# Optimization experiments

Hardware: AMD Instinct MI355X
Metric: run time of the kernel (lower is better)

The kernel has to match this reference:

```python
import jax, jax.numpy as jnp
import numpy as np

N_SIDE = 14          # ViT-S/16 on 224x224 -> 14x14 patches
D_BACKBONE = 384
D_MODEL = 512
B_CLIPS = 32
T_FRAMES = 64
BT = B_CLIPS * T_FRAMES
LN_EPS = 1e-5


def setup_inputs() -> dict:
    key = jax.random.key(0)
    k0, k1, k2, k3, k4 = jax.random.split(key, 5)
    patch_tokens = jax.random.normal(k0, (BT, N_SIDE * N_SIDE, D_BACKBONE), dtype=jnp.float32)
    raw = jax.random.uniform(k1, (BT, 4), dtype=jnp.float32)
    # make well-formed boxes: x1<=x2, y1<=y2 (module clamps anyway)
    xy1 = jnp.minimum(raw[:, :2], raw[:, 2:])
    xy2 = jnp.maximum(raw[:, :2], raw[:, 2:])
    bboxes = jnp.concatenate([xy1, xy2], axis=1)
    obj_visible = jax.random.bernoulli(k2, 0.9, (BT,)).astype(jnp.float32)
    W = jax.random.normal(k3, (D_BACKBONE, D_MODEL), dtype=jnp.float32) * 0.02
    b = jnp.zeros((D_MODEL,), dtype=jnp.float32)
    gamma = jnp.ones((D_MODEL,), dtype=jnp.float32)
    beta = jnp.zeros((D_MODEL,), dtype=jnp.float32)
    mask_token = jax.random.normal(k4, (1, D_MODEL), dtype=jnp.float32) * 0.02
    return {"patch_tokens": patch_tokens, "bboxes": bboxes, "obj_visible": obj_visible,
            "B": B_CLIPS, "T": T_FRAMES, "W": W, "b": b, "gamma": gamma, "beta": beta,
            "mask_token": mask_token}


def _roi_mean_pool(patch_tokens, bboxes):
    bt, N, D = patch_tokens.shape
    n = N_SIDE
    grid = patch_tokens.reshape(bt, n, n, D)
    # exact replica of torch index math (clamp -> trunc/ceil -> clamp -> max)
    x1 = jnp.clip(bboxes[:, 0] * n, 0, n - 1).astype(jnp.int32)
    y1 = jnp.clip(bboxes[:, 1] * n, 0, n - 1).astype(jnp.int32)
    x2 = jnp.clip(jnp.ceil(jnp.clip(bboxes[:, 2] * n, 0, n)), 1, n).astype(jnp.int32)
    y2 = jnp.clip(jnp.ceil(jnp.clip(bboxes[:, 3] * n, 0, n)), 1, n).astype(jnp.int32)
    x2 = jnp.maximum(x2, x1 + 1)
    y2 = jnp.maximum(y2, y1 + 1)
    idx = jnp.arange(n)
    my = (idx[None, :] >= y1[:, None]) & (idx[None, :] < y2[:, None])  # [BT, n]
    mx = (idx[None, :] >= x1[:, None]) & (idx[None, :] < x2[:, None])  # [BT, n]
    mask = (my[:, :, None] & mx[:, None, :]).astype(grid.dtype)        # [BT, n, n]
    count = ((y2 - y1) * (x2 - x1)).astype(grid.dtype)                 # >= 1 always
    pooled = jnp.einsum('bhw,bhwd->bd', mask, grid) / count[:, None]
    return pooled


def reference(patch_tokens, bboxes, obj_visible, B, T, W, b, gamma, beta, mask_token):
    pooled = _roi_mean_pool(patch_tokens, bboxes)          # [BT, D_backbone]
    out = pooled @ W + b                                   # [BT, d_model]
    mu = jnp.mean(out, axis=-1, keepdims=True)
    var = jnp.mean(jnp.square(out - mu), axis=-1, keepdims=True)
    out = (out - mu) * jax.lax.rsqrt(var + LN_EPS) * gamma + beta
    vis = obj_visible[:, None]
    out = vis * out + (1.0 - vis) * mask_token             # learnable mask token blend
    return out.reshape(B, T, -1)
```

## Files before the change

kernel.cpp:

```cpp
#include <hip/hip_runtime.h>
#include <hip/hip_bf16.h>

#define N_SIDE 14
#define N_PATCH (N_SIDE * N_SIDE)
#define D_BB 384
#define DQ_BB (D_BB / 4)
#define D_MODEL 512
#define CQ (D_MODEL / 4)
#define BT_TOTAL 2048
#define LN_EPS 1e-5f
#define ROWS 8
#define KP 4
#define KCHUNK (D_BB / KP)
#define GROUPS 8

__device__ __forceinline__ void fma4(float4& a, float s, const float4& wv) {
    a.x = fmaf(s, wv.x, a.x);
    a.y = fmaf(s, wv.y, a.y);
    a.z = fmaf(s, wv.z, a.z);
    a.w = fmaf(s, wv.w, a.w);
}

__global__ __launch_bounds__(768) void pool_kernel(
    const float* __restrict__ patch,
    const float* __restrict__ bboxes,
    float* __restrict__ pooled)
{
    const int bt = blockIdx.x;
    const int t  = threadIdx.x;
    const int qd = t % DQ_BB;
    const int g  = t / DQ_BB;

    const float bx1 = bboxes[bt * 4 + 0];
    const float by1 = bboxes[bt * 4 + 1];
    const float bx2 = bboxes[bt * 4 + 2];
    const float by2 = bboxes[bt * 4 + 3];

    int x1 = (int)fminf(fmaxf(bx1 * (float)N_SIDE, 0.f), (float)(N_SIDE - 1));
    int y1 = (int)fminf(fmaxf(by1 * (float)N_SIDE, 0.f), (float)(N_SIDE - 1));
    int x2 = (int)fminf(fmaxf(ceilf(fminf(fmaxf(bx2 * (float)N_SIDE, 0.f), (float)N_SIDE)), 1.f), (float)N_SIDE);
    int y2 = (int)fminf(fmaxf(ceilf(fminf(fmaxf(by2 * (float)N_SIDE, 0.f), (float)N_SIDE)), 1.f), (float)N_SIDE);
    x2 = max(x2, x1 + 1);
    y2 = max(y2, y1 + 1);

    const int wd = x2 - x1;
    const int ht = y2 - y1;
    const int total = wd * ht;
    const float inv_count = 1.f / (float)total;
    const float inv_wd = 1.f / (float)wd;
    const int cell0 = y1 * N_SIDE + x1;

    const float4* __restrict__ base = (const float4*)patch + (size_t)bt * N_PATCH * DQ_BB + qd;

    auto cell_off = [&](int c) -> size_t {
        const int y = (int)(((float)c + 0.5f) * inv_wd);
        const int x = c - y * wd;
        return (size_t)(cell0 + y * N_SIDE + x) * DQ_BB;
    };

    float4 acc = make_float4(0.f, 0.f, 0.f, 0.f);
    int c = g;
    for (; c + 3 * GROUPS < total; c += 4 * GROUPS) {
        const float4 v0 = base[cell_off(c)];
        const float4 v1 = base[cell_off(c + GROUPS)];
        const float4 v2 = base[cell_off(c + 2 * GROUPS)];
        const float4 v3 = base[cell_off(c + 3 * GROUPS)];
        acc.x += (v0.x + v1.x) + (v2.x + v3.x);
        acc.y += (v0.y + v1.y) + (v2.y + v3.y);
        acc.z += (v0.z + v1.z) + (v2.z + v3.z);
        acc.w += (v0.w + v1.w) + (v2.w + v3.w);
    }
    for (; c < total; c += GROUPS) {
        const float4 v = base[cell_off(c)];
        acc.x += v.x; acc.y += v.y; acc.z += v.z; acc.w += v.w;
    }

    __shared__ float4 part[GROUPS][DQ_BB];
    part[g][qd] = acc;
    __syncthreads();

    if (t < DQ_BB) {
        float4 s = part[0][t];
#pragma unroll
        for (int p = 1; p < GROUPS; ++p) {
            const float4 v = part[p][t];
            s.x += v.x; s.y += v.y; s.z += v.z; s.w += v.w;
        }
        s.x *= inv_count; s.y *= inv_count; s.z *= inv_count; s.w *= inv_count;
        ((float4*)pooled)[(size_t)bt * DQ_BB + t] = s;
    }
}

__global__ __launch_bounds__(512) void gemm_ln_kernel(
    const float* __restrict__ pooled,
    const float* __restrict__ W,
    const float* __restrict__ bias,
    const float* __restrict__ gamma,
    const float* __restrict__ beta,
    const float* __restrict__ mask_tok,
    const float* __restrict__ vis,
    float* __restrict__ out)
{
    const int tid  = threadIdx.x;
    const int part = tid >> 7;
    const int jq   = tid & 127;
    const int r0   = blockIdx.x * ROWS;

    __shared__ float sp[ROWS][D_BB];
    __shared__ float red[KP - 1][32][CQ];
    __shared__ float lnred[2][ROWS][2];

    {
        const float4* p4  = (const float4*)(pooled + (size_t)r0 * D_BB);
        float4*       sp4 = (float4*)sp;
        for (int i = tid; i < ROWS * DQ_BB; i += 512) sp4[i] = p4[i];
    }
    __syncthreads();

    const float4* Wq = (const float4*)W;
    float4 acc[ROWS];
#pragma unroll
    for (int r = 0; r < ROWS; ++r) acc[r] = make_float4(0.f, 0.f, 0.f, 0.f);

    const int dbase = part * KCHUNK;
#pragma unroll 2
    for (int i = 0; i < KCHUNK / 4; ++i) {
        const int d = dbase + i * 4;
        const float4 w0 = Wq[(size_t)(d + 0) * CQ + jq];
        const float4 w1 = Wq[(size_t)(d + 1) * CQ + jq];
        const float4 w2 = Wq[(size_t)(d + 2) * CQ + jq];
        const float4 w3 = Wq[(size_t)(d + 3) * CQ + jq];
#pragma unroll
        for (int r = 0; r < ROWS; ++r) {
            const float4 a = *(const float4*)&sp[r][d];
            fma4(acc[r], a.x, w0);
            fma4(acc[r], a.y, w1);
            fma4(acc[r], a.z, w2);
            fma4(acc[r], a.w, w3);
        }
    }

    if (part != 0) {
#pragma unroll
        for (int r = 0; r < ROWS; ++r) {
            red[part - 1][r * 4 + 0][jq] = acc[r].x;
            red[part - 1][r * 4 + 1][jq] = acc[r].y;
            red[part - 1][r * 4 + 2][jq] = acc[r].z;
            red[part - 1][r * 4 + 3][jq] = acc[r].w;
        }
    }
    __syncthreads();

    if (part == 0) {
#pragma unroll
        for (int p = 0; p < KP - 1; ++p) {
#pragma unroll
            for (int r = 0; r < ROWS; ++r) {
                acc[r].x += red[p][r * 4 + 0][jq];
                acc[r].y += red[p][r * 4 + 1][jq];
                acc[r].z += red[p][r * 4 + 2][jq];
                acc[r].w += red[p][r * 4 + 3][jq];
            }
        }
        const float4 bj = ((const float4*)bias)[jq];
#pragma unroll
        for (int r = 0; r < ROWS; ++r) {
            acc[r].x += bj.x; acc[r].y += bj.y; acc[r].z += bj.z; acc[r].w += bj.w;
        }

        const int lane = tid & 63;
        const int wv   = tid >> 6;
#pragma unroll
        for (int r = 0; r < ROWS; ++r) {
            float s  = acc[r].x + acc[r].y + acc[r].z + acc[r].w;
            float s2 = acc[r].x * acc[r].x + acc[r].y * acc[r].y +
                       acc[r].z * acc[r].z + acc[r].w * acc[r].w;
#pragma unroll
            for (int off = 32; off >= 1; off >>= 1) {
                s  += __shfl_xor(s,  off);
                s2 += __shfl_xor(s2, off);
            }
            if (lane == 0) { lnred[wv][r][0] = s; lnred[wv][r][1] = s2; }
        }
    }
    __syncthreads();

    if (part == 0) {
        const float4 g4 = ((const float4*)gamma)[jq];
        const float4 b4 = ((const float4*)beta)[jq];
        const float4 m4 = ((const float4*)mask_tok)[jq];
#pragma unroll
        for (int r = 0; r < ROWS; ++r) {
            const float s    = lnred[0][r][0] + lnred[1][r][0];
            const float s2   = lnred[0][r][1] + lnred[1][r][1];
            const float mean = s * (1.f / (float)D_MODEL);
            const float var  = s2 * (1.f / (float)D_MODEL) - mean * mean;
            const float rstd = rsqrtf(var + LN_EPS);
            const float v    = vis[r0 + r];
            const float iv   = 1.f - v;
            float4 o;
            o.x = v * ((acc[r].x - mean) * rstd * g4.x + b4.x) + iv * m4.x;
            o.y = v * ((acc[r].y - mean) * rstd * g4.y + b4.y) + iv * m4.y;
            o.z = v * ((acc[r].z - mean) * rstd * g4.z + b4.z) + iv * m4.z;
            o.w = v * ((acc[r].w - mean) * rstd * g4.w + b4.w) + iv * m4.w;
            ((float4*)out)[(size_t)(r0 + r) * CQ + jq] = o;
        }
    }
}

extern "C" void kernel_launch(void* const* d_in, const int* in_sizes, int n_in,
                              void* d_out, int out_size, void* d_ws, size_t ws_size,
                              hipStream_t stream) {
    const float* patch  = (const float*)d_in[0];
    const float* bboxes = (const float*)d_in[1];
    const float* vis    = (const float*)d_in[2];
    const float* W      = (const float*)d_in[5];
    const float* bias   = (const float*)d_in[6];
    const float* gamma  = (const float*)d_in[7];
    const float* beta   = (const float*)d_in[8];
    const float* mtok   = (const float*)d_in[9];

    float* pooled = (float*)d_ws;
    float* out    = (float*)d_out;

    pool_kernel<<<BT_TOTAL, 768, 0, stream>>>(patch, bboxes, pooled);
    gemm_ln_kernel<<<BT_TOTAL / ROWS, 512, 0, stream>>>(
        pooled, W, bias, gamma, beta, mtok, vis, out);
}
```

Before: 37.68 us.

## Split ROI pooling across two blocks per box with atomic accumulation

Each box's pooling is now spread over two 384-thread blocks instead of one 768-thread block. The partial sums are combined with float atomicAdd into a workspace that is zeroed by a memset first. The division by the cell count moves into the GEMM+LayerNorm epilogue, which recomputes the box size. The aim is finer-grained scheduling, at the cost of an extra memset launch, atomic traffic, and summation order that is no longer deterministic.

```diff
diff --git a/kernel.cpp b/kernel.cpp
--- a/kernel.cpp
+++ b/kernel.cpp
@@ -12,7 +12,9 @@
 #define ROWS 8
 #define KP 4
 #define KCHUNK (D_BB / KP)
-#define GROUPS 8
+#define GROUPS 4
+#define SPLIT 2
+#define ESTRIDE (GROUPS * SPLIT)
 
 __device__ __forceinline__ void fma4(float4& a, float s, const float4& wv) {
     a.x = fmaf(s, wv.x, a.x);
@@ -21,32 +23,37 @@
     a.w = fmaf(s, wv.w, a.w);
 }
 
-__global__ __launch_bounds__(768) void pool_kernel(
+__device__ __forceinline__ void box_params(const float* __restrict__ bboxes, int bt,
+                                           int& x1, int& y1, int& wd, int& total) {
+    const float bx1 = bboxes[bt * 4 + 0];
+    const float by1 = bboxes[bt * 4 + 1];
+    const float bx2 = bboxes[bt * 4 + 2];
+    const float by2 = bboxes[bt * 4 + 3];
+    x1 = (int)fminf(fmaxf(bx1 * (float)N_SIDE, 0.f), (float)(N_SIDE - 1));
+    y1 = (int)fminf(fmaxf(by1 * (float)N_SIDE, 0.f), (float)(N_SIDE - 1));
+    int x2 = (int)fminf(fmaxf(ceilf(fminf(fmaxf(bx2 * (float)N_SIDE, 0.f), (float)N_SIDE)), 1.f), (float)N_SIDE);
+    int y2 = (int)fminf(fmaxf(ceilf(fminf(fmaxf(by2 * (float)N_SIDE, 0.f), (float)N_SIDE)), 1.f), (float)N_SIDE);
+    x2 = max(x2, x1 + 1);
+    y2 = max(y2, y1 + 1);
+    wd = x2 - x1;
+    total = wd * (y2 - y1);
+}
+
+__global__ __launch_bounds__(384) void pool_kernel(
     const float* __restrict__ patch,
     const float* __restrict__ bboxes,
     float* __restrict__ pooled)
 {
-    const int bt = blockIdx.x;
-    const int t  = threadIdx.x;
-    const int qd = t % DQ_BB;
-    const int g  = t / DQ_BB;
-
-    const float bx1 = bboxes[bt * 4 + 0];
-    const float by1 = bboxes[bt * 4 + 1];
-    const float bx2 = bboxes[bt * 4 + 2];
-    const float by2 = bboxes[bt * 4 + 3];
-
-    int x1 = (int)fminf(fmaxf(bx1 * (float)N_SIDE, 0.f), (float)(N_SIDE - 1));
-    int y1 = (int)fminf(fmaxf(by1 * (float)N_SIDE, 0.f), (float)(N_SIDE - 1));
-    int x2 = (int)fminf(fmaxf(ceilf(fminf(fmaxf(bx2 * (float)N_SIDE, 0.f), (float)N_SIDE)), 1.f), (float)N_SIDE);
-    int y2 = (int)fminf(fmaxf(ceilf(fminf(fmaxf(by2 * (float)N_SIDE, 0.f), (float)N_SIDE)), 1.f), (float)N_SIDE);
-    x2 = max(x2, x1 + 1);
-    y2 = max(y2, y1 + 1);
-
-    const int wd = x2 - x1;
-    const int ht = y2 - y1;
-    const int total = wd * ht;
-    const float inv_count = 1.f / (float)total;
+    const int bid = blockIdx.x;
+    const int bt  = bid >> 1;
+    const int s   = bid & 1;
+    const int t   = threadIdx.x;
+    const int qd  = t % DQ_BB;
+    const int g   = t / DQ_BB;
+    const int e   = s * GROUPS + g;
+
+    int x1, y1, wd, total;
+    box_params(bboxes, bt, x1, y1, wd, total);
     const float inv_wd = 1.f / (float)wd;
     const int cell0 = y1 * N_SIDE + x1;
 
@@ -59,18 +66,18 @@
     };
 
     float4 acc = make_float4(0.f, 0.f, 0.f, 0.f);
-    int c = g;
-    for (; c + 3 * GROUPS < total; c += 4 * GROUPS) {
+    int c = e;
+    for (; c + 3 * ESTRIDE < total; c += 4 * ESTRIDE) {
         const float4 v0 = base[cell_off(c)];
-        const float4 v1 = base[cell_off(c + GROUPS)];
-        const float4 v2 = base[cell_off(c + 2 * GROUPS)];
-        const float4 v3 = base[cell_off(c + 3 * GROUPS)];
+        const float4 v1 = base[cell_off(c + ESTRIDE)];
+        const float4 v2 = base[cell_off(c + 2 * ESTRIDE)];
+        const float4 v3 = base[cell_off(c + 3 * ESTRIDE)];
         acc.x += (v0.x + v1.x) + (v2.x + v3.x);
         acc.y += (v0.y + v1.y) + (v2.y + v3.y);
         acc.z += (v0.z + v1.z) + (v2.z + v3.z);
         acc.w += (v0.w + v1.w) + (v2.w + v3.w);
     }
-    for (; c < total; c += GROUPS) {
+    for (; c < total; c += ESTRIDE) {
         const float4 v = base[cell_off(c)];
         acc.x += v.x; acc.y += v.y; acc.z += v.z; acc.w += v.w;
     }
@@ -80,19 +87,23 @@
     __syncthreads();
 
     if (t < DQ_BB) {
-        float4 s = part[0][t];
+        float4 sm = part[0][t];
 #pragma unroll
         for (int p = 1; p < GROUPS; ++p) {
             const float4 v = part[p][t];
-            s.x += v.x; s.y += v.y; s.z += v.z; s.w += v.w;
-        }
-        s.x *= inv_count; s.y *= inv_count; s.z *= inv_count; s.w *= inv_count;
-        ((float4*)pooled)[(size_t)bt * DQ_BB + t] = s;
+            sm.x += v.x; sm.y += v.y; sm.z += v.z; sm.w += v.w;
+        }
+        float* dst = pooled + (size_t)bt * D_BB + t * 4;
+        atomicAdd(dst + 0, sm.x);
+        atomicAdd(dst + 1, sm.y);
+        atomicAdd(dst + 2, sm.z);
+        atomicAdd(dst + 3, sm.w);
     }
 }
 
 __global__ __launch_bounds__(512) void gemm_ln_kernel(
     const float* __restrict__ pooled,
+    const float* __restrict__ bboxes,
     const float* __restrict__ W,
     const float* __restrict__ bias,
     const float* __restrict__ gamma,
@@ -109,11 +120,17 @@
     __shared__ float sp[ROWS][D_BB];
     __shared__ float red[KP - 1][32][CQ];
     __shared__ float lnred[2][ROWS][2];
+    __shared__ float s_invc[ROWS];
 
     {
         const float4* p4  = (const float4*)(pooled + (size_t)r0 * D_BB);
         float4*       sp4 = (float4*)sp;
         for (int i = tid; i < ROWS * DQ_BB; i += 512) sp4[i] = p4[i];
+    }
+    if (tid < ROWS) {
+        int x1, y1, wd, total;
+        box_params(bboxes, r0 + tid, x1, y1, wd, total);
+        s_invc[tid] = 1.f / (float)total;
     }
     __syncthreads();
 
@@ -165,7 +182,11 @@
         const float4 bj = ((const float4*)bias)[jq];
 #pragma unroll
         for (int r = 0; r < ROWS; ++r) {
-            acc[r].x += bj.x; acc[r].y += bj.y; acc[r].z += bj.z; acc[r].w += bj.w;
+            const float ic = s_invc[r];
+            acc[r].x = fmaf(acc[r].x, ic, bj.x);
+            acc[r].y = fmaf(acc[r].y, ic, bj.y);
+            acc[r].z = fmaf(acc[r].z, ic, bj.z);
+            acc[r].w = fmaf(acc[r].w, ic, bj.w);
         }
 
         const int lane = tid & 63;
@@ -223,7 +244,8 @@
     float* pooled = (float*)d_ws;
     float* out    = (float*)d_out;
 
-    pool_kernel<<<BT_TOTAL, 768, 0, stream>>>(patch, bboxes, pooled);
+    hipMemsetAsync(pooled, 0, (size_t)BT_TOTAL * D_BB * sizeof(float), stream);
+    pool_kernel<<<BT_TOTAL * SPLIT, 384, 0, stream>>>(patch, bboxes, pooled);
     gemm_ln_kernel<<<BT_TOTAL / ROWS, 512, 0, stream>>>(
-        pooled, W, bias, gamma, beta, mtok, vis, out);
-}
+        pooled, bboxes, W, bias, gamma, beta, mtok, vis, out);
+}
```

After: 53.41 us. 41.8% more time.
